# Performance work log

Measured on AMD Instinct MI355X. Metric: run time of the kernel, lower is better.

The kernel has to match this reference:

```python
import jax, jax.numpy as jnp
import numpy as np
import math

B, S, D = 4, 2048, 1024


def setup_inputs() -> dict:
    key = jax.random.key(0)
    k1, k2, k3 = jax.random.split(key, 3)
    X = jax.random.normal(k1, (B, S, D), dtype=jnp.float32)
    # causal mask, broadcast over batch (True = keep)
    mask = jnp.broadcast_to(jnp.tril(jnp.ones((S, S), dtype=bool)), (B, S, S))
    # torch nn.Linear weights: y = x @ W.T; init scale ~ 1/sqrt(D)
    WQK = jax.random.normal(k2, (D, D), dtype=jnp.float32) / math.sqrt(D)
    WOV = jax.random.normal(k3, (D, D), dtype=jnp.float32) / math.sqrt(D)
    return {"X": X, "mask": mask, "WQK": WQK, "WOV": WOV}


def reference(X, mask, WQK, WOV):
    d = X.shape[-1]
    Q = jnp.einsum('bsd,ed->bse', X, WQK)          # WQK(X) = X @ WQK.T
    Sc = jnp.einsum('bse,bte->bst', Q, X)          # shared-QK scores: Q @ X^T
    # NOTE: original multiplies by sqrt(d_model) (not divide) - faithful
    Sc = Sc * jnp.asarray(math.sqrt(d), Sc.dtype)
    Sc = jnp.where(mask, Sc, -jnp.inf)
    A = jax.nn.softmax(Sc, axis=-1)                # dropout p=0.0 -> identity
    V = jnp.einsum('bsd,ed->bse', X, WOV)          # WOV(X)
    Y = jnp.einsum('bst,bte->bse', A, V)
    return (X + Y, A)
```

## Files before the change

### kernel.cpp

```cpp
#include <hip/hip_runtime.h>
#include <hip/hip_fp16.h>
#include <math.h>

typedef _Float16 half_t;
typedef _Float16 h8_t __attribute__((ext_vector_type(8)));
typedef _Float16 h4_t __attribute__((ext_vector_type(4)));
typedef float f4_t __attribute__((ext_vector_type(4)));

#define MFMA16(a, b, c) __builtin_amdgcn_mfma_f32_16x16x32_f16(a, b, c, 0, 0, 0)

static constexpr int kB = 4;
static constexpr int kS = 2048;
static constexpr int kD = 1024;
static constexpr int BM = 128;
static constexpr int BN = 128;
static constexpr int BK = 32;
static constexpr int LDK = BK + 8;

__device__ __forceinline__ void stage_tile(half_t* __restrict__ sm,
                                           const half_t* __restrict__ g, int ld) {
  const int t = threadIdx.x;
  const int r = t >> 2;
  const int c = (t & 3) * 8;
  *(h8_t*)&sm[r * LDK + c]        = *(const h8_t*)&g[(size_t)r * ld + c];
  *(h8_t*)&sm[(r + 64) * LDK + c] = *(const h8_t*)&g[(size_t)(r + 64) * ld + c];
}

template <bool SPLIT>
__device__ __forceinline__ void gemm_core(const half_t* __restrict__ Ahi,
                                          const half_t* __restrict__ Alo, int lda,
                                          const half_t* __restrict__ Bhi,
                                          const half_t* __restrict__ Blo, int ldb,
                                          int k_iters, half_t* sm, f4_t acc[4][4]) {
  half_t* sAh = sm;
  half_t* sBh = sm + BM * LDK;
  half_t* sAl = sm + 2 * BM * LDK;
  half_t* sBl = sm + 3 * BM * LDK;
  const int lane = threadIdx.x & 63;
  const int wid = threadIdx.x >> 6;
  const int wm = (wid >> 1) * 64;
  const int wn = (wid & 1) * 64;
  const int fr = lane & 15;
  const int fk = (lane >> 4) * 8;

  for (int kk = 0; kk < k_iters; ++kk) {
    const size_t ko = (size_t)kk * BK;
    stage_tile(sAh, Ahi + ko, lda);
    stage_tile(sBh, Bhi + ko, ldb);
    if (SPLIT) {
      stage_tile(sAl, Alo + ko, lda);
      stage_tile(sBl, Blo + ko, ldb);
    }
    __syncthreads();
    h8_t a[4], b[4], al[4], bl[4];
#pragma unroll
    for (int i = 0; i < 4; ++i) {
      a[i] = *(h8_t*)&sAh[(wm + i * 16 + fr) * LDK + fk];
      b[i] = *(h8_t*)&sBh[(wn + i * 16 + fr) * LDK + fk];
      if (SPLIT) {
        al[i] = *(h8_t*)&sAl[(wm + i * 16 + fr) * LDK + fk];
        bl[i] = *(h8_t*)&sBl[(wn + i * 16 + fr) * LDK + fk];
      }
    }
#pragma unroll
    for (int i = 0; i < 4; ++i)
#pragma unroll
      for (int j = 0; j < 4; ++j) {
        acc[i][j] = MFMA16(a[i], b[j], acc[i][j]);
        if (SPLIT) {
          acc[i][j] = MFMA16(a[i], bl[j], acc[i][j]);
          acc[i][j] = MFMA16(al[i], b[j], acc[i][j]);
        }
      }
    __syncthreads();
  }
}

__global__ __launch_bounds__(256) void gemm_q_kernel(
    const half_t* __restrict__ Xhi, const half_t* __restrict__ Xlo,
    const half_t* __restrict__ Whi, const half_t* __restrict__ Wlo,
    half_t* __restrict__ Qhi, half_t* __restrict__ Qlo) {
  __shared__ half_t sm[4 * BM * LDK];
  const size_t arow = (size_t)blockIdx.y * BM;
  const size_t brow = (size_t)blockIdx.x * BN;
  f4_t acc[4][4] = {};
  gemm_core<true>(Xhi + arow * kD, Xlo + arow * kD, kD,
                  Whi + brow * kD, Wlo + brow * kD, kD, kD / BK, sm, acc);
  const int lane = threadIdx.x & 63;
  const int wid = threadIdx.x >> 6;
  const int wm = (wid >> 1) * 64, wn = (wid & 1) * 64;
  const int c16 = lane & 15, r4 = (lane >> 4) * 4;
#pragma unroll
  for (int i = 0; i < 4; ++i)
#pragma unroll
    for (int j = 0; j < 4; ++j)
#pragma unroll
      for (int r = 0; r < 4; ++r) {
        const size_t row = arow + wm + i * 16 + r4 + r;
        const size_t col = brow + wn + j * 16 + c16;
        const float q = acc[i][j][r];
        const half_t qh = (half_t)q;
        const half_t ql = (half_t)(q - (float)qh);
        const size_t idx = row * kD + col;
        Qhi[idx] = qh;
        Qlo[idx] = ql;
      }
}

__global__ __launch_bounds__(256) void gemm_v_kernel(
    const half_t* __restrict__ Xhi, const half_t* __restrict__ Whi,
    half_t* __restrict__ Vt) {
  __shared__ half_t sm[2 * BM * LDK];
  const size_t arow = (size_t)blockIdx.y * BM;
  const size_t brow = (size_t)blockIdx.x * BN;
  f4_t acc[4][4] = {};
  gemm_core<false>(Xhi + arow * kD, nullptr, kD, Whi + brow * kD, nullptr, kD,
                   kD / BK, sm, acc);
  const int lane = threadIdx.x & 63;
  const int wid = threadIdx.x >> 6;
  const int wm = (wid >> 1) * 64, wn = (wid & 1) * 64;
  const int c16 = lane & 15, r4 = (lane >> 4) * 4;
#pragma unroll
  for (int i = 0; i < 4; ++i)
#pragma unroll
    for (int j = 0; j < 4; ++j)
#pragma unroll
      for (int r = 0; r < 4; ++r) {
        const size_t row = arow + wm + i * 16 + r4 + r;
        const size_t col = brow + wn + j * 16 + c16;
        const size_t bi = row >> 11;
        const size_t s = row & 2047;
        Vt[bi * (size_t)kD * kS + col * kS + s] = (half_t)acc[i][j][r];
      }
}

__global__ __launch_bounds__(256) void gemm_score_kernel(
    const half_t* __restrict__ Qhi, const half_t* __restrict__ Qlo,
    const half_t* __restrict__ Xhi, const half_t* __restrict__ Xlo,
    float* __restrict__ Sc) {
  const int tn = blockIdx.x, tm = blockIdx.y, bi = blockIdx.z;
  if (tn > tm) return;
  __shared__ half_t sm[4 * BM * LDK];
  const size_t arow = (size_t)bi * kS + (size_t)tm * BM;
  const size_t brow = (size_t)bi * kS + (size_t)tn * BN;
  f4_t acc[4][4] = {};
  gemm_core<true>(Qhi + arow * kD, Qlo + arow * kD, kD,
                  Xhi + brow * kD, Xlo + brow * kD, kD, kD / BK, sm, acc);
  float* out = Sc + (size_t)bi * kS * kS;
  const int lane = threadIdx.x & 63;
  const int wid = threadIdx.x >> 6;
  const int wm = (wid >> 1) * 64, wn = (wid & 1) * 64;
  const int c16 = lane & 15, r4 = (lane >> 4) * 4;
#pragma unroll
  for (int i = 0; i < 4; ++i)
#pragma unroll
    for (int j = 0; j < 4; ++j)
#pragma unroll
      for (int r = 0; r < 4; ++r) {
        const int row = tm * BM + wm + i * 16 + r4 + r;
        const int col = tn * BN + wn + j * 16 + c16;
        out[(size_t)row * kS + col] = 32.0f * acc[i][j][r];
      }
}

__global__ __launch_bounds__(256) void softmax_kernel(float* __restrict__ A,
                                                      half_t* __restrict__ Ah) {
  const int rgl = blockIdx.x;
  const int s = rgl & 2047;
  float* row = A + (size_t)rgl * kS;
  half_t* hrow = Ah + (size_t)rgl * kS;
  const int tid = threadIdx.x;
  const int n = s + 1;
  float v[8];
  float mx = -INFINITY;
#pragma unroll
  for (int i = 0; i < 8; ++i) {
    const int t = tid + i * 256;
    v[i] = (t < n) ? row[t] : -INFINITY;
    mx = fmaxf(mx, v[i]);
  }
  for (int off = 32; off; off >>= 1) mx = fmaxf(mx, __shfl_xor(mx, off));
  __shared__ float red[8];
  const int lane = tid & 63, wid = tid >> 6;
  if (lane == 0) red[wid] = mx;
  __syncthreads();
  if (tid == 0) {
    float m = fmaxf(fmaxf(red[0], red[1]), fmaxf(red[2], red[3]));
    red[4] = m;
  }
  __syncthreads();
  mx = red[4];
  float sum = 0.0f;
#pragma unroll
  for (int i = 0; i < 8; ++i) {
    v[i] = (tid + i * 256 < n) ? __expf(v[i] - mx) : 0.0f;
    sum += v[i];
  }
  for (int off = 32; off; off >>= 1) sum += __shfl_xor(sum, off);
  __syncthreads();
  if (lane == 0) red[wid] = sum;
  __syncthreads();
  if (tid == 0) red[5] = 1.0f / (red[0] + red[1] + red[2] + red[3]);
  __syncthreads();
  const float inv = red[5];
#pragma unroll
  for (int i = 0; i < 8; ++i) {
    const int t = tid + i * 256;
    const float a = v[i] * inv;
    row[t] = a;
    hrow[t] = (half_t)a;
  }
}

__global__ __launch_bounds__(256) void gemm_y_kernel(
    const half_t* __restrict__ Ah, const half_t* __restrict__ Vt,
    const float* __restrict__ X, float* __restrict__ Out) {
  __shared__ half_t sm[2 * BM * LDK];
  const int tn = blockIdx.x, tm = blockIdx.y, bi = blockIdx.z;
  const size_t abase = ((size_t)bi * kS + (size_t)tm * BM) * kS;
  const size_t bbase = ((size_t)bi * kD + (size_t)tn * BN) * kS;
  f4_t acc[4][4] = {};
  gemm_core<false>(Ah + abase, nullptr, kS, Vt + bbase, nullptr, kS,
                   (tm + 1) * BM / BK, sm, acc);
  const size_t obase = (size_t)bi * kS * kD;
  const int lane = threadIdx.x & 63;
  const int wid = threadIdx.x >> 6;
  const int wm = (wid >> 1) * 64, wn = (wid & 1) * 64;
  const int c16 = lane & 15, r4 = (lane >> 4) * 4;
#pragma unroll
  for (int i = 0; i < 4; ++i)
#pragma unroll
    for (int j = 0; j < 4; ++j)
#pragma unroll
      for (int r = 0; r < 4; ++r) {
        const size_t row = (size_t)tm * BM + wm + i * 16 + r4 + r;
        const size_t col = (size_t)tn * BN + wn + j * 16 + c16;
        const size_t idx = obase + row * kD + col;
        Out[idx] = X[idx] + acc[i][j][r];
      }
}

__global__ __launch_bounds__(256) void split_kernel(const float* __restrict__ x,
                                                    half_t* __restrict__ hi,
                                                    half_t* __restrict__ lo, int n4) {
  const int i = blockIdx.x * 256 + threadIdx.x;
  if (i >= n4) return;
  const float4 v = ((const float4*)x)[i];
  const float vv[4] = {v.x, v.y, v.z, v.w};
  h4_t h, l;
#pragma unroll
  for (int j = 0; j < 4; ++j) {
    const half_t hh = (half_t)vv[j];
    h[j] = hh;
    l[j] = (half_t)(vv[j] - (float)hh);
  }
  ((h4_t*)hi)[i] = h;
  ((h4_t*)lo)[i] = l;
}

__global__ __launch_bounds__(256) void cvt_kernel(const float* __restrict__ x,
                                                  half_t* __restrict__ hi, int n4) {
  const int i = blockIdx.x * 256 + threadIdx.x;
  if (i >= n4) return;
  const float4 v = ((const float4*)x)[i];
  h4_t h;
  h[0] = (half_t)v.x; h[1] = (half_t)v.y; h[2] = (half_t)v.z; h[3] = (half_t)v.w;
  ((h4_t*)hi)[i] = h;
}

extern "C" void kernel_launch(void* const* d_in, const int* in_sizes, int n_in,
                              void* d_out, int out_size, void* d_ws, size_t ws_size,
                              hipStream_t stream) {
  const float* X   = (const float*)d_in[0];
  const float* WQK = (const float*)d_in[2];
  const float* WOV = (const float*)d_in[3];

  constexpr size_t nX = (size_t)kB * kS * kD;
  constexpr size_t nW = (size_t)kD * kD;
  constexpr size_t nA = (size_t)kB * kS * kS;

  float* out0 = (float*)d_out;
  float* outA = out0 + nX;

  half_t* ws = (half_t*)d_ws;
  half_t* Xhi = ws; ws += nX;
  half_t* Xlo = ws; ws += nX;
  half_t* Qhi = ws; ws += nX;
  half_t* Qlo = ws; ws += nX;
  half_t* Whi = ws; ws += nW;
  half_t* Wlo = ws; ws += nW;
  half_t* WVh = ws; ws += nW;
  half_t* Vt  = ws; ws += nX;
  half_t* Ah  = ws; ws += nA;
  const size_t need_bytes = (size_t)((char*)ws - (char*)d_ws);
  if (ws_size < need_bytes) return;

  split_kernel<<<(int)(nX / 4 / 256), 256, 0, stream>>>(X, Xhi, Xlo, (int)(nX / 4));
  split_kernel<<<(int)(nW / 4 / 256), 256, 0, stream>>>(WQK, Whi, Wlo, (int)(nW / 4));
  cvt_kernel<<<(int)(nW / 4 / 256), 256, 0, stream>>>(WOV, WVh, (int)(nW / 4));

  gemm_q_kernel<<<dim3(kD / BN, kB * kS / BM), 256, 0, stream>>>(Xhi, Xlo, Whi, Wlo, Qhi, Qlo);
  gemm_v_kernel<<<dim3(kD / BN, kB * kS / BM), 256, 0, stream>>>(Xhi, WVh, Vt);
  gemm_score_kernel<<<dim3(kS / BN, kS / BM, kB), 256, 0, stream>>>(Qhi, Qlo, Xhi, Xlo, outA);
  softmax_kernel<<<kB * kS, 256, 0, stream>>>(outA, Ah);
  gemm_y_kernel<<<dim3(kD / BN, kS / BM, kB), 256, 0, stream>>>(Ah, Vt, X, out0);
}
```

Baseline: 431.0 us.

## Stage GEMM tiles via direct global-to-LDS loads with k-chunk-major layout

Replaces the register-staged global→LDS tile copies in the shared GEMM core with __builtin_amdgcn_global_load_lds 16-byte direct loads. The shared-memory tile layout changes from padded row-major (LDK=40) to a k-chunk-major layout where each wave fills one 8-half k-slice for 128 rows, and fragment reads index it accordingly. This is meant to remove VGPR round-trips and issue overhead for staging and to shrink LDS per block. The cost is uncoalesced-ish global access per lane (each lane reads a different row), reliance on correct wait/sync semantics for the async LDS loads, and possible new LDS bank patterns on fragment reads.

```diff
diff --git a/kernel.cpp b/kernel.cpp
--- a/kernel.cpp
+++ b/kernel.cpp
@@ -6,6 +6,7 @@
 typedef _Float16 h8_t __attribute__((ext_vector_type(8)));
 typedef _Float16 h4_t __attribute__((ext_vector_type(4)));
 typedef float f4_t __attribute__((ext_vector_type(4)));
+typedef unsigned int u32;
 
 #define MFMA16(a, b, c) __builtin_amdgcn_mfma_f32_16x16x32_f16(a, b, c, 0, 0, 0)
 
@@ -15,15 +16,12 @@
 static constexpr int BM = 128;
 static constexpr int BN = 128;
 static constexpr int BK = 32;
-static constexpr int LDK = BK + 8;
-
-__device__ __forceinline__ void stage_tile(half_t* __restrict__ sm,
-                                           const half_t* __restrict__ g, int ld) {
-  const int t = threadIdx.x;
-  const int r = t >> 2;
-  const int c = (t & 3) * 8;
-  *(h8_t*)&sm[r * LDK + c]        = *(const h8_t*)&g[(size_t)r * ld + c];
-  *(h8_t*)&sm[(r + 64) * LDK + c] = *(const h8_t*)&g[(size_t)(r + 64) * ld + c];
+static constexpr int TILE_H = 4096;
+
+__device__ __forceinline__ void gld16(const half_t* g, half_t* l) {
+  __builtin_amdgcn_global_load_lds(
+      (const __attribute__((address_space(1))) u32*)g,
+      (__attribute__((address_space(3))) u32*)l, 16, 0, 0);
 }
 
 template <bool SPLIT>
@@ -33,33 +31,52 @@
                                           const half_t* __restrict__ Blo, int ldb,
                                           int k_iters, half_t* sm, f4_t acc[4][4]) {
   half_t* sAh = sm;
-  half_t* sBh = sm + BM * LDK;
-  half_t* sAl = sm + 2 * BM * LDK;
-  half_t* sBl = sm + 3 * BM * LDK;
+  half_t* sBh = sm + TILE_H;
+  half_t* sAl = sm + 2 * TILE_H;
+  half_t* sBl = sm + 3 * TILE_H;
   const int lane = threadIdx.x & 63;
   const int wid = threadIdx.x >> 6;
   const int wm = (wid >> 1) * 64;
   const int wn = (wid & 1) * 64;
   const int fr = lane & 15;
-  const int fk = (lane >> 4) * 8;
+  const int quad = lane >> 4;
+
+  const size_t ga0 = (size_t)lane * lda + wid * 8;
+  const size_t ga1 = ga0 + (size_t)64 * lda;
+  const size_t gb0 = (size_t)lane * ldb + wid * 8;
+  const size_t gb1 = gb0 + (size_t)64 * ldb;
+  half_t* lA0 = sAh + wid * 1024;
+  half_t* lA1 = lA0 + 512;
+  half_t* lB0 = sBh + wid * 1024;
+  half_t* lB1 = lB0 + 512;
+  half_t* lAl0 = sAl + wid * 1024;
+  half_t* lAl1 = lAl0 + 512;
+  half_t* lBl0 = sBl + wid * 1024;
+  half_t* lBl1 = lBl0 + 512;
+
+  const int fbase = quad * 1024 + fr * 8;
 
   for (int kk = 0; kk < k_iters; ++kk) {
     const size_t ko = (size_t)kk * BK;
-    stage_tile(sAh, Ahi + ko, lda);
-    stage_tile(sBh, Bhi + ko, ldb);
+    gld16(Ahi + ko + ga0, lA0);
+    gld16(Ahi + ko + ga1, lA1);
+    gld16(Bhi + ko + gb0, lB0);
+    gld16(Bhi + ko + gb1, lB1);
     if (SPLIT) {
-      stage_tile(sAl, Alo + ko, lda);
-      stage_tile(sBl, Blo + ko, ldb);
+      gld16(Alo + ko + ga0, lAl0);
+      gld16(Alo + ko + ga1, lAl1);
+      gld16(Blo + ko + gb0, lBl0);
+      gld16(Blo + ko + gb1, lBl1);
     }
     __syncthreads();
     h8_t a[4], b[4], al[4], bl[4];
 #pragma unroll
     for (int i = 0; i < 4; ++i) {
-      a[i] = *(h8_t*)&sAh[(wm + i * 16 + fr) * LDK + fk];
-      b[i] = *(h8_t*)&sBh[(wn + i * 16 + fr) * LDK + fk];
+      a[i] = *(h8_t*)&sAh[fbase + (wm + i * 16) * 8];
+      b[i] = *(h8_t*)&sBh[fbase + (wn + i * 16) * 8];
       if (SPLIT) {
-        al[i] = *(h8_t*)&sAl[(wm + i * 16 + fr) * LDK + fk];
-        bl[i] = *(h8_t*)&sBl[(wn + i * 16 + fr) * LDK + fk];
+        al[i] = *(h8_t*)&sAl[fbase + (wm + i * 16) * 8];
+        bl[i] = *(h8_t*)&sBl[fbase + (wn + i * 16) * 8];
       }
     }
 #pragma unroll
@@ -80,7 +97,7 @@
     const half_t* __restrict__ Xhi, const half_t* __restrict__ Xlo,
     const half_t* __restrict__ Whi, const half_t* __restrict__ Wlo,
     half_t* __restrict__ Qhi, half_t* __restrict__ Qlo) {
-  __shared__ half_t sm[4 * BM * LDK];
+  __shared__ half_t sm[4 * TILE_H];
   const size_t arow = (size_t)blockIdx.y * BM;
   const size_t brow = (size_t)blockIdx.x * BN;
   f4_t acc[4][4] = {};
@@ -110,7 +127,7 @@
 __global__ __launch_bounds__(256) void gemm_v_kernel(
     const half_t* __restrict__ Xhi, const half_t* __restrict__ Whi,
     half_t* __restrict__ Vt) {
-  __shared__ half_t sm[2 * BM * LDK];
+  __shared__ half_t sm[2 * TILE_H];
   const size_t arow = (size_t)blockIdx.y * BM;
   const size_t brow = (size_t)blockIdx.x * BN;
   f4_t acc[4][4] = {};
@@ -140,7 +157,7 @@
     float* __restrict__ Sc) {
   const int tn = blockIdx.x, tm = blockIdx.y, bi = blockIdx.z;
   if (tn > tm) return;
-  __shared__ half_t sm[4 * BM * LDK];
+  __shared__ half_t sm[4 * TILE_H];
   const size_t arow = (size_t)bi * kS + (size_t)tm * BM;
   const size_t brow = (size_t)bi * kS + (size_t)tn * BN;
   f4_t acc[4][4] = {};
@@ -215,7 +232,7 @@
 __global__ __launch_bounds__(256) void gemm_y_kernel(
     const half_t* __restrict__ Ah, const half_t* __restrict__ Vt,
     const float* __restrict__ X, float* __restrict__ Out) {
-  __shared__ half_t sm[2 * BM * LDK];
+  __shared__ half_t sm[2 * TILE_H];
   const int tn = blockIdx.x, tm = blockIdx.y, bi = blockIdx.z;
   const size_t abase = ((size_t)bi * kS + (size_t)tm * BM) * kS;
   const size_t bbase = ((size_t)bi * kD + (size_t)tn * BN) * kS;
```

After: 485.7 us. 12.7% more time.

## Use 256x128 tiles, register-prefetch pipeline, and XCD-aware causal block scheduling

Applied to the files above, without the earlier changes.

Grows GEMM tiles to 256x128 with 512 threads. Global loads for the next K-step are prefetched into registers during the current step. The shared-memory layout changes to k-block-major with no padding. Grid launches are flattened with a custom tile mapping: the causal score tiles are enumerated explicitly, and the light and heavy rows of the triangle are paired so each block group gets balanced work. This is meant to raise data reuse and hide load latency, at the cost of more registers and possible LDS bank conflicts from the unpadded layout.

```diff
diff --git a/kernel.cpp b/kernel.cpp
--- a/kernel.cpp
+++ b/kernel.cpp
@@ -12,19 +12,9 @@
 static constexpr int kB = 4;
 static constexpr int kS = 2048;
 static constexpr int kD = 1024;
-static constexpr int BM = 128;
+static constexpr int BM = 256;
 static constexpr int BN = 128;
 static constexpr int BK = 32;
-static constexpr int LDK = BK + 8;
-
-__device__ __forceinline__ void stage_tile(half_t* __restrict__ sm,
-                                           const half_t* __restrict__ g, int ld) {
-  const int t = threadIdx.x;
-  const int r = t >> 2;
-  const int c = (t & 3) * 8;
-  *(h8_t*)&sm[r * LDK + c]        = *(const h8_t*)&g[(size_t)r * ld + c];
-  *(h8_t*)&sm[(r + 64) * LDK + c] = *(const h8_t*)&g[(size_t)(r + 64) * ld + c];
-}
 
 template <bool SPLIT>
 __device__ __forceinline__ void gemm_core(const half_t* __restrict__ Ahi,
@@ -33,33 +23,66 @@
                                           const half_t* __restrict__ Blo, int ldb,
                                           int k_iters, half_t* sm, f4_t acc[4][4]) {
   half_t* sAh = sm;
-  half_t* sBh = sm + BM * LDK;
-  half_t* sAl = sm + 2 * BM * LDK;
-  half_t* sBl = sm + 3 * BM * LDK;
-  const int lane = threadIdx.x & 63;
-  const int wid = threadIdx.x >> 6;
-  const int wm = (wid >> 1) * 64;
-  const int wn = (wid & 1) * 64;
+  half_t* sBh = sm + 8192;
+  half_t* sAl = sm + 12288;
+  half_t* sBl = sm + 20480;
+  const int t = threadIdx.x;
+  const int lane = t & 63;
+  const int wid = t >> 6;
+  const int wm = (wid & 3) * 64;
+  const int wn = (wid >> 2) * 64;
   const int fr = lane & 15;
-  const int fk = (lane >> 4) * 8;
+  const int quad = lane >> 4;
+  const int rowA = t & 255, kbA = t >> 8;
+  const int rowB = t & 127, kbB = t >> 7;
+  const size_t gA1 = (size_t)rowA * lda + kbA * 8;
+  const size_t gA2 = gA1 + 16;
+  const size_t gB  = (size_t)rowB * ldb + kbB * 8;
+  const int lA1 = kbA * 2048 + rowA * 8;
+  const int lA2 = lA1 + 2 * 2048;
+  const int lB  = kbB * 1024 + rowB * 8;
+  const int fA = quad * 2048 + fr * 8;
+  const int fB = quad * 1024 + fr * 8;
+
+  h8_t rA1, rA2, rB1, rAl1, rAl2, rBl1;
+  rA1 = *(const h8_t*)&Ahi[gA1];
+  rA2 = *(const h8_t*)&Ahi[gA2];
+  rB1 = *(const h8_t*)&Bhi[gB];
+  if constexpr (SPLIT) {
+    rAl1 = *(const h8_t*)&Alo[gA1];
+    rAl2 = *(const h8_t*)&Alo[gA2];
+    rBl1 = *(const h8_t*)&Blo[gB];
+  }
 
   for (int kk = 0; kk < k_iters; ++kk) {
-    const size_t ko = (size_t)kk * BK;
-    stage_tile(sAh, Ahi + ko, lda);
-    stage_tile(sBh, Bhi + ko, ldb);
-    if (SPLIT) {
-      stage_tile(sAl, Alo + ko, lda);
-      stage_tile(sBl, Blo + ko, ldb);
+    *(h8_t*)&sAh[lA1] = rA1;
+    *(h8_t*)&sAh[lA2] = rA2;
+    *(h8_t*)&sBh[lB] = rB1;
+    if constexpr (SPLIT) {
+      *(h8_t*)&sAl[lA1] = rAl1;
+      *(h8_t*)&sAl[lA2] = rAl2;
+      *(h8_t*)&sBl[lB] = rBl1;
     }
     __syncthreads();
+    if (kk + 1 < k_iters) {
+      const size_t ko = (size_t)(kk + 1) * BK;
+      rA1 = *(const h8_t*)&Ahi[gA1 + ko];
+      rA2 = *(const h8_t*)&Ahi[gA2 + ko];
+      rB1 = *(const h8_t*)&Bhi[gB + ko];
+      if constexpr (SPLIT) {
+        rAl1 = *(const h8_t*)&Alo[gA1 + ko];
+        rAl2 = *(const h8_t*)&Alo[gA2 + ko];
+        rBl1 = *(const h8_t*)&Blo[gB + ko];
+      }
+    }
     h8_t a[4], b[4], al[4], bl[4];
 #pragma unroll
     for (int i = 0; i < 4; ++i) {
-      a[i] = *(h8_t*)&sAh[(wm + i * 16 + fr) * LDK + fk];
-      b[i] = *(h8_t*)&sBh[(wn + i * 16 + fr) * LDK + fk];
-      if (SPLIT) {
-        al[i] = *(h8_t*)&sAl[(wm + i * 16 + fr) * LDK + fk];
-        bl[i] = *(h8_t*)&sBl[(wn + i * 16 + fr) * LDK + fk];
+      a[i] = *(h8_t*)&sAh[fA + (wm + i * 16) * 8];
+      b[i] = *(h8_t*)&sBh[fB + (wn + i * 16) * 8];
+      if constexpr (SPLIT) {
+        al[i] = *(h8_t*)&sAl[fA + (wm + i * 16) * 8];
+        bl[i] = *(h8_t*)&sBl[fB + (wn + i * 16) * 8];
       }
     }
 #pragma unroll
@@ -67,7 +90,7 @@
 #pragma unroll
       for (int j = 0; j < 4; ++j) {
         acc[i][j] = MFMA16(a[i], b[j], acc[i][j]);
-        if (SPLIT) {
+        if constexpr (SPLIT) {
           acc[i][j] = MFMA16(a[i], bl[j], acc[i][j]);
           acc[i][j] = MFMA16(al[i], b[j], acc[i][j]);
         }
@@ -76,19 +99,21 @@
   }
 }
 
-__global__ __launch_bounds__(256) void gemm_q_kernel(
+__global__ __launch_bounds__(512, 1) void gemm_q_kernel(
     const half_t* __restrict__ Xhi, const half_t* __restrict__ Xlo,
     const half_t* __restrict__ Whi, const half_t* __restrict__ Wlo,
     half_t* __restrict__ Qhi, half_t* __restrict__ Qlo) {
-  __shared__ half_t sm[4 * BM * LDK];
-  const size_t arow = (size_t)blockIdx.y * BM;
-  const size_t brow = (size_t)blockIdx.x * BN;
+  __shared__ half_t sm[24576];
+  const int x = blockIdx.x & 7, s = blockIdx.x >> 3;
+  const int mi = x + 8 * (s >> 3), ni = s & 7;
+  const size_t arow = (size_t)mi * BM;
+  const size_t brow = (size_t)ni * BN;
   f4_t acc[4][4] = {};
   gemm_core<true>(Xhi + arow * kD, Xlo + arow * kD, kD,
                   Whi + brow * kD, Wlo + brow * kD, kD, kD / BK, sm, acc);
   const int lane = threadIdx.x & 63;
   const int wid = threadIdx.x >> 6;
-  const int wm = (wid >> 1) * 64, wn = (wid & 1) * 64;
+  const int wm = (wid & 3) * 64, wn = (wid >> 2) * 64;
   const int c16 = lane & 15, r4 = (lane >> 4) * 4;
 #pragma unroll
   for (int i = 0; i < 4; ++i)
@@ -98,27 +123,29 @@
       for (int r = 0; r < 4; ++r) {
         const size_t row = arow + wm + i * 16 + r4 + r;
         const size_t col = brow + wn + j * 16 + c16;
-        const float q = acc[i][j][r];
-        const half_t qh = (half_t)q;
-        const half_t ql = (half_t)(q - (float)qh);
+        const float qv = acc[i][j][r];
+        const half_t qh = (half_t)qv;
+        const half_t ql = (half_t)(qv - (float)qh);
         const size_t idx = row * kD + col;
         Qhi[idx] = qh;
         Qlo[idx] = ql;
       }
 }
 
-__global__ __launch_bounds__(256) void gemm_v_kernel(
+__global__ __launch_bounds__(512, 1) void gemm_v_kernel(
     const half_t* __restrict__ Xhi, const half_t* __restrict__ Whi,
     half_t* __restrict__ Vt) {
-  __shared__ half_t sm[2 * BM * LDK];
-  const size_t arow = (size_t)blockIdx.y * BM;
-  const size_t brow = (size_t)blockIdx.x * BN;
+  __shared__ half_t sm[12288];
+  const int x = blockIdx.x & 7, s = blockIdx.x >> 3;
+  const int mi = x + 8 * (s >> 3), ni = s & 7;
+  const size_t arow = (size_t)mi * BM;
+  const size_t brow = (size_t)ni * BN;
   f4_t acc[4][4] = {};
   gemm_core<false>(Xhi + arow * kD, nullptr, kD, Whi + brow * kD, nullptr, kD,
                    kD / BK, sm, acc);
   const int lane = threadIdx.x & 63;
   const int wid = threadIdx.x >> 6;
-  const int wm = (wid >> 1) * 64, wn = (wid & 1) * 64;
+  const int wm = (wid & 3) * 64, wn = (wid >> 2) * 64;
   const int c16 = lane & 15, r4 = (lane >> 4) * 4;
 #pragma unroll
   for (int i = 0; i < 4; ++i)
@@ -129,37 +156,48 @@
         const size_t row = arow + wm + i * 16 + r4 + r;
         const size_t col = brow + wn + j * 16 + c16;
         const size_t bi = row >> 11;
-        const size_t s = row & 2047;
-        Vt[bi * (size_t)kD * kS + col * kS + s] = (half_t)acc[i][j][r];
-      }
-}
-
-__global__ __launch_bounds__(256) void gemm_score_kernel(
+        const size_t ss = row & 2047;
+        Vt[bi * (size_t)kD * kS + col * kS + ss] = (half_t)acc[i][j][r];
+      }
+}
+
+__global__ __launch_bounds__(512, 1) void gemm_score_kernel(
     const half_t* __restrict__ Qhi, const half_t* __restrict__ Qlo,
     const half_t* __restrict__ Xhi, const half_t* __restrict__ Xlo,
     float* __restrict__ Sc) {
-  const int tn = blockIdx.x, tm = blockIdx.y, bi = blockIdx.z;
-  if (tn > tm) return;
-  __shared__ half_t sm[4 * BM * LDK];
-  const size_t arow = (size_t)bi * kS + (size_t)tm * BM;
-  const size_t brow = (size_t)bi * kS + (size_t)tn * BN;
+  const int x = blockIdx.x & 7;
+  const int s = blockIdx.x >> 3;
+  const int c = (s < 18) ? x : x + 8;
+  const int j = (s < 18) ? s : s - 18;
+  const int bi = c >> 2, p = c & 3;
+  int m, n;
+  if (j < 4 * p + 4) {
+    n = j >> 1;
+    m = (j & 1) ? 7 - p : p;
+  } else {
+    n = j - 2 * p - 2;
+    m = 7 - p;
+  }
+  __shared__ half_t sm[24576];
+  const size_t arow = (size_t)bi * kS + (size_t)m * BM;
+  const size_t brow = (size_t)bi * kS + (size_t)n * BN;
   f4_t acc[4][4] = {};
   gemm_core<true>(Qhi + arow * kD, Qlo + arow * kD, kD,
                   Xhi + brow * kD, Xlo + brow * kD, kD, kD / BK, sm, acc);
   float* out = Sc + (size_t)bi * kS * kS;
   const int lane = threadIdx.x & 63;
   const int wid = threadIdx.x >> 6;
-  const int wm = (wid >> 1) * 64, wn = (wid & 1) * 64;
+  const int wm = (wid & 3) * 64, wn = (wid >> 2) * 64;
   const int c16 = lane & 15, r4 = (lane >> 4) * 4;
 #pragma unroll
   for (int i = 0; i < 4; ++i)
 #pragma unroll
-    for (int j = 0; j < 4; ++j)
+    for (int jj = 0; jj < 4; ++jj)
 #pragma unroll
       for (int r = 0; r < 4; ++r) {
-        const int row = tm * BM + wm + i * 16 + r4 + r;
-        const int col = tn * BN + wn + j * 16 + c16;
-        out[(size_t)row * kS + col] = 32.0f * acc[i][j][r];
+        const int row = m * BM + wm + i * 16 + r4 + r;
+        const int col = n * BN + wn + jj * 16 + c16;
+        out[(size_t)row * kS + col] = 32.0f * acc[i][jj][r];
       }
 }
 
@@ -185,8 +223,8 @@
   if (lane == 0) red[wid] = mx;
   __syncthreads();
   if (tid == 0) {
-    float m = fmaxf(fmaxf(red[0], red[1]), fmaxf(red[2], red[3]));
-    red[4] = m;
+    float mm = fmaxf(fmaxf(red[0], red[1]), fmaxf(red[2], red[3]));
+    red[4] = mm;
   }
   __syncthreads();
   mx = red[4];
@@ -212,20 +250,22 @@
   }
 }
 
-__global__ __launch_bounds__(256) void gemm_y_kernel(
+__global__ __launch_bounds__(512, 1) void gemm_y_kernel(
     const half_t* __restrict__ Ah, const half_t* __restrict__ Vt,
     const float* __restrict__ X, float* __restrict__ Out) {
-  __shared__ half_t sm[2 * BM * LDK];
-  const int tn = blockIdx.x, tm = blockIdx.y, bi = blockIdx.z;
-  const size_t abase = ((size_t)bi * kS + (size_t)tm * BM) * kS;
-  const size_t bbase = ((size_t)bi * kD + (size_t)tn * BN) * kS;
+  const int x = blockIdx.x & 7, s = blockIdx.x >> 3;
+  const int bi = s >> 3, n = s & 7;
+  const int m = (bi & 1) ? (7 - x) : x;
+  __shared__ half_t sm[12288];
+  const size_t abase = ((size_t)bi * kS + (size_t)m * BM) * kS;
+  const size_t bbase = ((size_t)bi * kD + (size_t)n * BN) * kS;
   f4_t acc[4][4] = {};
   gemm_core<false>(Ah + abase, nullptr, kS, Vt + bbase, nullptr, kS,
-                   (tm + 1) * BM / BK, sm, acc);
+                   (m + 1) * BM / BK, sm, acc);
   const size_t obase = (size_t)bi * kS * kD;
   const int lane = threadIdx.x & 63;
   const int wid = threadIdx.x >> 6;
-  const int wm = (wid >> 1) * 64, wn = (wid & 1) * 64;
+  const int wm = (wid & 3) * 64, wn = (wid >> 2) * 64;
   const int c16 = lane & 15, r4 = (lane >> 4) * 4;
 #pragma unroll
   for (int i = 0; i < 4; ++i)
@@ -233,8 +273,8 @@
     for (int j = 0; j < 4; ++j)
 #pragma unroll
       for (int r = 0; r < 4; ++r) {
-        const size_t row = (size_t)tm * BM + wm + i * 16 + r4 + r;
-        const size_t col = (size_t)tn * BN + wn + j * 16 + c16;
+        const size_t row = (size_t)m * BM + wm + i * 16 + r4 + r;
+        const size_t col = (size_t)n * BN + wn + j * 16 + c16;
         const size_t idx = obase + row * kD + col;
         Out[idx] = X[idx] + acc[i][j][r];
       }
@@ -299,9 +339,9 @@
   split_kernel<<<(int)(nW / 4 / 256), 256, 0, stream>>>(WQK, Whi, Wlo, (int)(nW / 4));
   cvt_kernel<<<(int)(nW / 4 / 256), 256, 0, stream>>>(WOV, WVh, (int)(nW / 4));
 
-  gemm_q_kernel<<<dim3(kD / BN, kB * kS / BM), 256, 0, stream>>>(Xhi, Xlo, Whi, Wlo, Qhi, Qlo);
-  gemm_v_kernel<<<dim3(kD / BN, kB * kS / BM), 256, 0, stream>>>(Xhi, WVh, Vt);
-  gemm_score_kernel<<<dim3(kS / BN, kS / BM, kB), 256, 0, stream>>>(Qhi, Qlo, Xhi, Xlo, outA);
+  gemm_q_kernel<<<256, 512, 0, stream>>>(Xhi, Xlo, Whi, Wlo, Qhi, Qlo);
+  gemm_v_kernel<<<256, 512, 0, stream>>>(Xhi, WVh, Vt);
+  gemm_score_kernel<<<288, 512, 0, stream>>>(Qhi, Qlo, Xhi, Xlo, outA);
   softmax_kernel<<<kB * kS, 256, 0, stream>>>(outA, Ah);
-  gemm_y_kernel<<<dim3(kD / BN, kS / BM, kB), 256, 0, stream>>>(Ah, Vt, X, out0);
-}
+  gemm_y_kernel<<<256, 512, 0, stream>>>(Ah, Vt, X, out0);
+}
```

Measured after the change: 506.7 us. 1.18x slower.
